# Kernel tuning notes

Hardware: AMD Instinct MI355X
Metric: run time of the kernel (lower is better)

## Reference

```python
import jax, jax.numpy as jnp
import numpy as np

N = 50000      # nodes
E = 400000     # edges (before self-loops)
IN = 128       # in_channels
OUT = 64       # out_channels (per-head; concat=False averages heads)
HEADS = 8      # heads of first GAT layer; second layer has 1 head
NEG_SLOPE = 0.2


def _glorot(key, shape, fan_in, fan_out):
    s = jnp.sqrt(2.0 / (fan_in + fan_out)).astype(jnp.float32)
    return jax.random.normal(key, shape, jnp.float32) * s


def setup_inputs() -> dict:
    key = jax.random.key(0)
    ks = jax.random.split(key, 10)
    x = jax.random.normal(ks[0], (N, IN), jnp.float32)
    edge_index = jax.random.randint(ks[1], (2, E), 0, N)
    # layer 1: heads=HEADS, per-head dim OUT
    W1 = _glorot(ks[2], (IN, HEADS * OUT), IN, HEADS * OUT)
    att_src1 = _glorot(ks[3], (HEADS, OUT), OUT, 1)
    att_dst1 = _glorot(ks[4], (HEADS, OUT), OUT, 1)
    b1 = jnp.zeros((OUT,), jnp.float32)
    # layer 2: heads=1
    W2 = _glorot(ks[5], (OUT, 1 * OUT), OUT, OUT)
    att_src2 = _glorot(ks[6], (1, OUT), OUT, 1)
    att_dst2 = _glorot(ks[7], (1, OUT), OUT, 1)
    b2 = jnp.zeros((OUT,), jnp.float32)
    return dict(x=x, edge_index=edge_index, W1=W1, att_src1=att_src1,
                att_dst1=att_dst1, b1=b1, W2=W2, att_src2=att_src2,
                att_dst2=att_dst2, b2=b2)


def gat_conv(x, edge_index, W, att_src, att_dst, bias, heads, ch):
    """PyG GATConv with concat=False (mean over heads), add_self_loops=True."""
    n = x.shape[0]
    loop = jnp.arange(n, dtype=edge_index.dtype)
    src = jnp.concatenate([edge_index[0], loop])  # [E+N]
    dst = jnp.concatenate([edge_index[1], loop])
    h = (x @ W).reshape(n, heads, ch)                     # [N, H, C]
    a_s = jnp.sum(h * att_src, axis=-1)                   # [N, H]
    a_d = jnp.sum(h * att_dst, axis=-1)                   # [N, H]
    e = jax.nn.leaky_relu(a_s[src] + a_d[dst], NEG_SLOPE)  # [E+N, H]
    # numerically stable segment softmax over incoming edges of each dst node
    emax = jax.lax.stop_gradient(
        jax.ops.segment_max(e, dst, num_segments=n))       # [N, H]
    ee = jnp.exp(e - emax[dst])
    denom = jax.ops.segment_sum(ee, dst, num_segments=n)  # [N, H]
    alpha = ee / denom[dst]                                # [E+N, H]
    out = jax.ops.segment_sum(alpha[:, :, None] * h[src], dst,
                              num_segments=n)              # [N, H, C]
    return out.mean(axis=1) + bias                         # [N, C]


def reference(x, edge_index, W1, att_src1, att_dst1, b1,
              W2, att_src2, att_dst2, b2):
    h = gat_conv(x, edge_index, W1, att_src1, att_dst1, b1, HEADS, OUT)
    h = jax.nn.elu(h)
    return gat_conv(h, edge_index, W2, att_src2, att_dst2, b2, 1, OUT)
```

## Files before the change

kernel.cpp:

```cpp
#include <hip/hip_runtime.h>
#include <cstdint>
#include <cstddef>

#define NEG_SLOPE 0.2f

typedef short bf16x8 __attribute__((ext_vector_type(8)));
typedef float f32x4 __attribute__((ext_vector_type(4)));
typedef float f32x2 __attribute__((ext_vector_type(2)));

__device__ __forceinline__ unsigned short f2bf(float f) {
  unsigned u = __float_as_uint(f);
  u = u + 0x7FFFu + ((u >> 16) & 1u);
  return (unsigned short)(u >> 16);
}
__device__ __forceinline__ float bf2f(unsigned short b) {
  return __uint_as_float((unsigned)b << 16);
}
__device__ __forceinline__ f32x2 unpk(unsigned xv) {
  f32x2 r;
  r.x = __uint_as_float(xv << 16);
  r.y = __uint_as_float(xv & 0xFFFF0000u);
  return r;
}
__device__ __forceinline__ void dma16(const unsigned short* g, unsigned short* l) {
  __builtin_amdgcn_global_load_lds(
      (const __attribute__((address_space(1))) unsigned*)g,
      (__attribute__((address_space(3))) unsigned*)l, 16, 0, 0);
}

__global__ __launch_bounds__(256) void prep_all(
    const int* __restrict__ ei, int* __restrict__ counts,
    const float* __restrict__ x, unsigned short* __restrict__ xb,
    const float* __restrict__ W1, const float* __restrict__ att_s1,
    const float* __restrict__ att_d1, unsigned short* __restrict__ AsAdT,
    unsigned short* __restrict__ WbT,
    const float* __restrict__ W2, unsigned short* __restrict__ W2t,
    const float* __restrict__ att_s2, const float* __restrict__ att_d2,
    float* __restrict__ AsAd2,
    int E, int ET, int N, int B0, int B1) {
  int b = blockIdx.x, tid = threadIdx.x;
  if (b < B0) {
    int i = b * 256 + tid;
    if (i < ET) {
      int dst = (i < E) ? ei[E + i] : (i - E);
      atomicAdd(&counts[dst], 1);
    }
    return;
  }
  b -= B0;
  if (b < B1) {
    int i = b * 256 + tid;
    if (i < N * 32) {
      float4 v = ((const float4*)x)[i];
      ushort4 o;
      o.x = f2bf(v.x); o.y = f2bf(v.y); o.z = f2bf(v.z); o.w = f2bf(v.w);
      ((ushort4*)xb)[i] = o;
    }
    return;
  }
  b -= B1;
  if (b < 8) {
    int i = b * 256 + tid;
    int o = i >> 7, k = i & 127, h = o & 7;
    const float* att = (o < 8) ? att_s1 : att_d1;
    float s = 0.f;
    for (int c = 0; c < 64; c++) s += W1[(size_t)k * 512 + h * 64 + c] * att[h * 64 + c];
    AsAdT[i] = f2bf(s);
    return;
  }
  b -= 8;
  if (b < 256) {
    int i = b * 256 + tid;
    int o = i >> 10, k = i & 1023, h = k >> 7, c = k & 127;
    WbT[i] = f2bf(W1[(size_t)c * 512 + h * 64 + o]);
    return;
  }
  b -= 256;
  if (b < 16) {
    int i = b * 256 + tid;
    if (i < 64 * 64) {
      int k = i >> 6, nn = i & 63;
      W2t[(size_t)nn * 64 + k] = f2bf(W2[i]);
    }
    return;
  }
  {
    int i = tid;
    if (i < 128) {
      int o = i >> 6, k = i & 63;
      const float* att = (o == 0) ? att_s2 : att_d2;
      float s = 0.f;
      for (int c = 0; c < 64; c++) s += W2[(size_t)k * 64 + c] * att[c];
      AsAd2[i] = s;
    }
  }
}

__global__ __launch_bounds__(1024) void scan_dots(
    const int* __restrict__ counts, int* __restrict__ offsets,
    const unsigned short* __restrict__ xb, const unsigned short* __restrict__ AsAdT,
    float* __restrict__ asd, int n) {
  if (blockIdx.x == 0) {
    __shared__ int sums[1024];
    int t = threadIdx.x;
    int chunk = (n + 1023) >> 10;
    int start = t * chunk;
    int end = min(start + chunk, n);
    int s = 0;
    for (int i = start; i < end; i++) s += counts[i];
    sums[t] = s;
    __syncthreads();
    for (int off = 1; off < 1024; off <<= 1) {
      int v = (t >= off) ? sums[t - off] : 0;
      __syncthreads();
      sums[t] += v;
      __syncthreads();
    }
    int run = sums[t] - s;
    for (int i = start; i < end; i++) { offsets[i] = run; run += counts[i]; }
    if (t == 1023) offsets[n] = sums[1023];
    return;
  }
  int tid = threadIdx.x;
  int wave = tid >> 6, lane = tid & 63;
  int q = lane >> 4, t = lane & 15;
  int row0 = (blockIdx.x - 1) * 256 + wave * 16;
  int arow = row0 + t; if (arow > n - 1) arow = n - 1;
  const bf16x8* aptr = (const bf16x8*)(xb + (size_t)arow * 128);
  const bf16x8* bptr = (const bf16x8*)(AsAdT + t * 128);
  f32x4 acc = (f32x4){0.f, 0.f, 0.f, 0.f};
  #pragma unroll
  for (int s = 0; s < 4; s++)
    acc = __builtin_amdgcn_mfma_f32_16x16x32_bf16(aptr[s * 4 + q], bptr[s * 4 + q],
                                                  acc, 0, 0, 0);
  #pragma unroll
  for (int r = 0; r < 4; r++) {
    int row = row0 + q * 4 + r;
    if (row < n) asd[row * 16 + t] = acc[r];
  }
}

__global__ __launch_bounds__(256) void fill_weights(
    const int* __restrict__ ei, const int* __restrict__ offsets,
    int* __restrict__ cursor, int* __restrict__ srcs,
    const float* __restrict__ asd, float* __restrict__ wbuf,
    int E, int ET) {
  int i = blockIdx.x * 256 + threadIdx.x;
  if (i >= ET) return;
  int src, dst;
  if (i < E) { src = ei[i]; dst = ei[E + i]; } else { src = dst = i - E; }
  int pos = atomicAdd(&cursor[dst], 1);
  int slot = offsets[dst] + pos;
  srcs[slot] = src;
  float4 s0 = *(const float4*)&asd[src * 16];
  float4 s1 = *(const float4*)&asd[src * 16 + 4];
  float4 d0 = *(const float4*)&asd[dst * 16 + 8];
  float4 d1 = *(const float4*)&asd[dst * 16 + 12];
  float w[8];
  w[0] = s0.x + d0.x; w[1] = s0.y + d0.y; w[2] = s0.z + d0.z; w[3] = s0.w + d0.w;
  w[4] = s1.x + d1.x; w[5] = s1.y + d1.y; w[6] = s1.z + d1.z; w[7] = s1.w + d1.w;
  #pragma unroll
  for (int h = 0; h < 8; h++) {
    float v = w[h];
    v = (v > 0.f) ? v : NEG_SLOPE * v;
    w[h] = __expf(v);
  }
  float4* wp = (float4*)&wbuf[(size_t)slot * 8];
  wp[0] = make_float4(w[0], w[1], w[2], w[3]);
  wp[1] = make_float4(w[4], w[5], w[6], w[7]);
}

__global__ __launch_bounds__(1024, 8) void agg1_gemm(
    const int* __restrict__ offsets, const int* __restrict__ srcs,
    const float* __restrict__ wbuf, const unsigned short* __restrict__ xb,
    const unsigned short* __restrict__ WbT, const float* __restrict__ b1,
    const float* __restrict__ AsAd2, unsigned short* __restrict__ zb,
    float* __restrict__ as2, float* __restrict__ ad2, int N) {
  __shared__ unsigned short sh[16 * 1032];
  __shared__ float sas[16], sad[16];
  int tid = threadIdx.x;
  int wv = tid >> 6, lane = tid & 63;
  int nb = blockIdx.x;
  {
    int row = wv;
    int node = nb * 16 + row;
    unsigned short* stg = &sh[row * 1032];
    f32x2 acc[8];
    float ws[8];
    #pragma unroll
    for (int h = 0; h < 8; h++) { acc[h] = (f32x2){0.f, 0.f}; ws[h] = 0.f; }
    int beg = offsets[node], end = offsets[node + 1];
    int jl = end - 1;
    int e0 = min(beg + (lane >> 4), jl);
    int e1 = min(beg + 4 + (lane >> 4), jl);
    int s0 = srcs[e0], s1 = srcs[e1];
    int we = min(beg + (lane >> 3), jl);
    float wl = wbuf[(size_t)we * 8 + (lane & 7)];
    for (int cb = beg; cb < end; cb += 8) {
      dma16(xb + (size_t)s0 * 128 + (lane & 15) * 8, stg);
      dma16(xb + (size_t)s1 * 128 + (lane & 15) * 8, stg + 512);
      float wcur = wl;
      int cn = cb + 8;
      int e0n = min(cn + (lane >> 4), jl);
      int e1n = min(cn + 4 + (lane >> 4), jl);
      s0 = srcs[e0n];
      s1 = srcs[e1n];
      int wen = min(cn + (lane >> 3), jl);
      wl = wbuf[(size_t)wen * 8 + (lane & 7)];
      __builtin_amdgcn_s_waitcnt(0x0f70);
      int cnt = min(8, end - cb);
      for (int k = 0; k < cnt; k++) {
        float w0 = __shfl(wcur, k * 8 + 0, 64);
        float w1 = __shfl(wcur, k * 8 + 1, 64);
        float w2 = __shfl(wcur, k * 8 + 2, 64);
        float w3 = __shfl(wcur, k * 8 + 3, 64);
        float w4 = __shfl(wcur, k * 8 + 4, 64);
        float w5 = __shfl(wcur, k * 8 + 5, 64);
        float w6 = __shfl(wcur, k * 8 + 6, 64);
        float w7 = __shfl(wcur, k * 8 + 7, 64);
        unsigned xv = *(const unsigned*)&stg[k * 128 + 2 * lane];
        f32x2 x2 = unpk(xv);
        acc[0] += x2 * w0; ws[0] += w0;
        acc[1] += x2 * w1; ws[1] += w1;
        acc[2] += x2 * w2; ws[2] += w2;
        acc[3] += x2 * w3; ws[3] += w3;
        acc[4] += x2 * w4; ws[4] += w4;
        acc[5] += x2 * w5; ws[5] += w5;
        acc[6] += x2 * w6; ws[6] += w6;
        acc[7] += x2 * w7; ws[7] += w7;
      }
    }
    #pragma unroll
    for (int h = 0; h < 8; h++) {
      float iv = 0.125f / ws[h];
      unsigned o = (unsigned)f2bf(acc[h].x * iv) | ((unsigned)f2bf(acc[h].y * iv) << 16);
      *(unsigned*)&sh[row * 1032 + h * 128 + 2 * lane] = o;
    }
  }
  if (tid < 16) sas[tid] = 0.f;
  else if (tid < 32) sad[tid - 16] = 0.f;
  __syncthreads();
  if (wv < 4) {
    int q = lane >> 4, t = lane & 15;
    f32x4 acc4 = (f32x4){0.f, 0.f, 0.f, 0.f};
    const unsigned short* bbase = WbT + (size_t)(wv * 16 + t) * 1024;
    #pragma unroll 8
    for (int s = 0; s < 32; s++) {
      bf16x8 af = *(const bf16x8*)&sh[t * 1032 + s * 32 + q * 8];
      bf16x8 bf = *(const bf16x8*)&bbase[s * 32 + q * 8];
      acc4 = __builtin_amdgcn_mfma_f32_16x16x32_bf16(af, bf, acc4, 0, 0, 0);
    }
    int col = wv * 16 + t;
    float bias = b1[col];
    float vs = AsAd2[col], vd = AsAd2[64 + col];
    float zr[4];
    #pragma unroll
    for (int r = 0; r < 4; r++) {
      int row = q * 4 + r;
      int node = nb * 16 + row;
      float v = acc4[r] + bias;
      v = (v > 0.f) ? v : (__expf(v) - 1.f);
      zr[r] = v;
      zb[(size_t)node * 64 + col] = f2bf(v);
    }
    #pragma unroll
    for (int r = 0; r < 4; r++) {
      float s = zr[r] * vs, d = zr[r] * vd;
      #pragma unroll
      for (int off = 1; off < 16; off <<= 1) {
        s += __shfl_xor(s, off, 64);
        d += __shfl_xor(d, off, 64);
      }
      if (t == 0) {
        atomicAdd(&sas[q * 4 + r], s);
        atomicAdd(&sad[q * 4 + r], d);
      }
    }
  }
  __syncthreads();
  if (tid < 16) as2[nb * 16 + tid] = sas[tid];
  else if (tid < 32) ad2[nb * 16 + (tid - 16)] = sad[tid - 16];
}

__global__ __launch_bounds__(1024, 8) void agg2_gemm(
    const int* __restrict__ offsets, const int* __restrict__ srcs,
    const float* __restrict__ as2, const float* __restrict__ ad2,
    const unsigned short* __restrict__ zb, const unsigned short* __restrict__ W2t,
    const float* __restrict__ b2, float* __restrict__ out, int N) {
  __shared__ unsigned short sh[16 * 72];
  __shared__ int ssrc[16][64];
  int tid = threadIdx.x;
  int wv = tid >> 6, lane = tid & 63;
  int nb = blockIdx.x;
  {
    int row = wv;
    int node = nb * 16 + row;
    int half = lane >> 5;
    int l2 = lane & 31;
    float adv = ad2[node];
    int beg = offsets[node], end = offsets[node + 1];
    f32x2 acc = (f32x2){0.f, 0.f};
    float ws = 0.f;
    for (int cb = beg; cb < end; cb += 64) {
      int cnt = min(64, end - cb);
      if (lane < cnt) ssrc[row][lane] = srcs[cb + lane];
      #pragma unroll 2
      for (int k = half; k < cnt; k += 2) {
        int s = ssrc[row][k];
        float asv = as2[s];
        unsigned zv = *(const unsigned*)&zb[(size_t)s * 64 + 2 * l2];
        float v = asv + adv;
        v = (v > 0.f) ? v : NEG_SLOPE * v;
        float w = __expf(v);
        ws += w;
        acc += unpk(zv) * w;
      }
    }
    acc.x += __shfl_xor(acc.x, 32, 64);
    acc.y += __shfl_xor(acc.y, 32, 64);
    ws += __shfl_xor(ws, 32, 64);
    if (half == 0) {
      float inv = 1.f / ws;
      unsigned o = (unsigned)f2bf(acc.x * inv) | ((unsigned)f2bf(acc.y * inv) << 16);
      *(unsigned*)&sh[row * 72 + 2 * l2] = o;
    }
  }
  __syncthreads();
  if (wv < 4) {
    int q = lane >> 4, t = lane & 15;
    f32x4 acc4 = (f32x4){0.f, 0.f, 0.f, 0.f};
    const unsigned short* bbase = W2t + (size_t)(wv * 16 + t) * 64;
    #pragma unroll
    for (int s = 0; s < 2; s++) {
      bf16x8 af = *(const bf16x8*)&sh[t * 72 + s * 32 + q * 8];
      bf16x8 bf = *(const bf16x8*)&bbase[s * 32 + q * 8];
      acc4 = __builtin_amdgcn_mfma_f32_16x16x32_bf16(af, bf, acc4, 0, 0, 0);
    }
    int col = wv * 16 + t;
    float bias = b2[col];
    #pragma unroll
    for (int r = 0; r < 4; r++) {
      int node = nb * 16 + q * 4 + r;
      if (node < N) out[(size_t)node * 64 + col] = acc4[r] + bias;
    }
  }
}

extern "C" void kernel_launch(void* const* d_in, const int* in_sizes, int n_in,
                              void* d_out, int out_size, void* d_ws, size_t ws_size,
                              hipStream_t stream) {
  const int IN = 128;
  const int N = in_sizes[0] / IN;
  const int E = in_sizes[1] / 2;
  const int ET = E + N;

  const float* x        = (const float*)d_in[0];
  const int*   ei       = (const int*)d_in[1];
  const float* W1       = (const float*)d_in[2];
  const float* att_src1 = (const float*)d_in[3];
  const float* att_dst1 = (const float*)d_in[4];
  const float* b1       = (const float*)d_in[5];
  const float* W2       = (const float*)d_in[6];
  const float* att_src2 = (const float*)d_in[7];
  const float* att_dst2 = (const float*)d_in[8];
  const float* b2       = (const float*)d_in[9];
  float* out = (float*)d_out;

  char* base = (char*)d_ws;
  size_t off = 0;
  auto alloc = [&](size_t bytes) -> char* {
    char* p = base + off;
    off = (off + bytes + 255) & ~(size_t)255;
    return p;
  };
  unsigned short* xb    = (unsigned short*)alloc((size_t)N * 128 * 2);
  unsigned short* AsAdT = (unsigned short*)alloc((size_t)16 * 128 * 2);
  unsigned short* WbT   = (unsigned short*)alloc((size_t)64 * 1024 * 2);
  unsigned short* W2t   = (unsigned short*)alloc((size_t)64 * 64 * 2);
  unsigned short* zb    = (unsigned short*)alloc((size_t)N * 64 * 2);
  float* AsAd2 = (float*)alloc((size_t)128 * 4);
  float* asd1  = (float*)alloc((size_t)N * 16 * 4);
  float* a_s2  = (float*)alloc((size_t)N * 4);
  float* a_d2  = (float*)alloc((size_t)N * 4);
  float* wbuf  = (float*)alloc((size_t)ET * 8 * 4);
  int* offsets = (int*)alloc((size_t)(N + 1) * 4);
  int* srcs    = (int*)alloc((size_t)ET * 4);
  char* zero_begin = base + off;
  int* counts  = (int*)alloc((size_t)N * 4);
  int* cursor  = (int*)alloc((size_t)N * 4);
  char* zero_end = base + off;

  hipMemsetAsync(zero_begin, 0, (size_t)(zero_end - zero_begin), stream);

  const int TB = 256;
  auto cdiv = [](int a, int b) { return (a + b - 1) / b; };

  int B0 = cdiv(ET, TB);
  int B1 = cdiv(N * 32, TB);
  prep_all<<<B0 + B1 + 8 + 256 + 16 + 1, TB, 0, stream>>>(
      ei, counts, x, xb, W1, att_src1, att_dst1, AsAdT, WbT, W2, W2t,
      att_src2, att_dst2, AsAd2, E, ET, N, B0, B1);

  scan_dots<<<1 + cdiv(N, 256), 1024, 0, stream>>>(counts, offsets, xb, AsAdT,
                                                   asd1, N);

  fill_weights<<<cdiv(ET, TB), TB, 0, stream>>>(ei, offsets, cursor, srcs,
                                                asd1, wbuf, E, ET);

  agg1_gemm<<<cdiv(N, 16), 1024, 0, stream>>>(offsets, srcs, wbuf, xb, WbT, b1,
                                              AsAd2, zb, a_s2, a_d2, N);

  agg2_gemm<<<cdiv(N, 16), 1024, 0, stream>>>(offsets, srcs, a_s2, a_d2, zb,
                                              W2t, b2, out, N);
}
```

Measured before the change: 339.7 us.

## Fuse edge-weight computation into layer-1 aggregation and process 16 edges per iteration

The per-edge attention weights (leaky-relu plus exp) are no longer precomputed and stored in a separate buffer. The layer-1 aggregation kernel now computes them on the fly from the per-node score table, so the weight buffer write and read disappear and the CSR fill kernel only scatters source indices. The aggregation loop now stages 16 neighbours per iteration through a larger shared buffer, broadcasts weights with readlane, and sums the softmax denominators with a final cross-lane reduction. Layer-2 scores are accumulated with global atomics into zeroed arrays instead of shared-memory atomics, and the larger shared allocation may lower occupancy.

```diff
diff --git a/kernel.cpp b/kernel.cpp
--- a/kernel.cpp
+++ b/kernel.cpp
@@ -21,6 +21,10 @@
   r.x = __uint_as_float(xv << 16);
   r.y = __uint_as_float(xv & 0xFFFF0000u);
   return r;
+}
+__device__ __forceinline__ float rlf(float v, int l) {
+  return __uint_as_float(
+      (unsigned)__builtin_amdgcn_readlane((int)__float_as_uint(v), l));
 }
 __device__ __forceinline__ void dma16(const unsigned short* g, unsigned short* l) {
   __builtin_amdgcn_global_load_lds(
@@ -140,105 +144,127 @@
   }
 }
 
-__global__ __launch_bounds__(256) void fill_weights(
+__global__ __launch_bounds__(256) void fill_csr(
     const int* __restrict__ ei, const int* __restrict__ offsets,
-    int* __restrict__ cursor, int* __restrict__ srcs,
-    const float* __restrict__ asd, float* __restrict__ wbuf,
-    int E, int ET) {
+    int* __restrict__ cursor, int* __restrict__ srcs, int E, int ET) {
   int i = blockIdx.x * 256 + threadIdx.x;
   if (i >= ET) return;
   int src, dst;
   if (i < E) { src = ei[i]; dst = ei[E + i]; } else { src = dst = i - E; }
   int pos = atomicAdd(&cursor[dst], 1);
-  int slot = offsets[dst] + pos;
-  srcs[slot] = src;
-  float4 s0 = *(const float4*)&asd[src * 16];
-  float4 s1 = *(const float4*)&asd[src * 16 + 4];
-  float4 d0 = *(const float4*)&asd[dst * 16 + 8];
-  float4 d1 = *(const float4*)&asd[dst * 16 + 12];
-  float w[8];
-  w[0] = s0.x + d0.x; w[1] = s0.y + d0.y; w[2] = s0.z + d0.z; w[3] = s0.w + d0.w;
-  w[4] = s1.x + d1.x; w[5] = s1.y + d1.y; w[6] = s1.z + d1.z; w[7] = s1.w + d1.w;
-  #pragma unroll
-  for (int h = 0; h < 8; h++) {
-    float v = w[h];
-    v = (v > 0.f) ? v : NEG_SLOPE * v;
-    w[h] = __expf(v);
-  }
-  float4* wp = (float4*)&wbuf[(size_t)slot * 8];
-  wp[0] = make_float4(w[0], w[1], w[2], w[3]);
-  wp[1] = make_float4(w[4], w[5], w[6], w[7]);
+  srcs[offsets[dst] + pos] = src;
 }
 
 __global__ __launch_bounds__(1024, 8) void agg1_gemm(
     const int* __restrict__ offsets, const int* __restrict__ srcs,
-    const float* __restrict__ wbuf, const unsigned short* __restrict__ xb,
+    const float* __restrict__ asd, const unsigned short* __restrict__ xb,
     const unsigned short* __restrict__ WbT, const float* __restrict__ b1,
     const float* __restrict__ AsAd2, unsigned short* __restrict__ zb,
     float* __restrict__ as2, float* __restrict__ ad2, int N) {
-  __shared__ unsigned short sh[16 * 1032];
-  __shared__ float sas[16], sad[16];
+  __shared__ unsigned short sh[16 * 2048];
   int tid = threadIdx.x;
   int wv = tid >> 6, lane = tid & 63;
   int nb = blockIdx.x;
   {
-    int row = wv;
-    int node = nb * 16 + row;
-    unsigned short* stg = &sh[row * 1032];
+    int node = nb * 16 + wv;
+    unsigned short* stg = &sh[wv * 2048];
     f32x2 acc[8];
-    float ws[8];
     #pragma unroll
-    for (int h = 0; h < 8; h++) { acc[h] = (f32x2){0.f, 0.f}; ws[h] = 0.f; }
+    for (int h = 0; h < 8; h++) acc[h] = (f32x2){0.f, 0.f};
+    float wsl = 0.f;
     int beg = offsets[node], end = offsets[node + 1];
     int jl = end - 1;
-    int e0 = min(beg + (lane >> 4), jl);
-    int e1 = min(beg + 4 + (lane >> 4), jl);
-    int s0 = srcs[e0], s1 = srcs[e1];
-    int we = min(beg + (lane >> 3), jl);
-    float wl = wbuf[(size_t)we * 8 + (lane & 7)];
-    for (int cb = beg; cb < end; cb += 8) {
+    float adv = asd[(size_t)node * 16 + 8 + (lane & 7)];
+    int s0 = srcs[min(beg + (lane >> 4), jl)];
+    int s1 = srcs[min(beg + 4 + (lane >> 4), jl)];
+    int s2 = 0, s3 = 0;
+    float asva, asvb = 0.f;
+    {
+      int swa = srcs[min(beg + (lane >> 3), jl)];
+      asva = asd[(size_t)swa * 16 + (lane & 7)];
+    }
+    if (end - beg > 8) {
+      s2 = srcs[min(beg + 8 + (lane >> 4), jl)];
+      s3 = srcs[min(beg + 12 + (lane >> 4), jl)];
+      int swb = srcs[min(beg + 8 + (lane >> 3), jl)];
+      asvb = asd[(size_t)swb * 16 + (lane & 7)];
+    }
+    for (int cb = beg; cb < end; cb += 16) {
+      int rem = end - cb;
+      bool bigh = rem > 8;
       dma16(xb + (size_t)s0 * 128 + (lane & 15) * 8, stg);
       dma16(xb + (size_t)s1 * 128 + (lane & 15) * 8, stg + 512);
-      float wcur = wl;
-      int cn = cb + 8;
-      int e0n = min(cn + (lane >> 4), jl);
-      int e1n = min(cn + 4 + (lane >> 4), jl);
-      s0 = srcs[e0n];
-      s1 = srcs[e1n];
-      int wen = min(cn + (lane >> 3), jl);
-      wl = wbuf[(size_t)wen * 8 + (lane & 7)];
+      if (bigh) {
+        dma16(xb + (size_t)s2 * 128 + (lane & 15) * 8, stg + 1024);
+        dma16(xb + (size_t)s3 * 128 + (lane & 15) * 8, stg + 1536);
+      }
+      float wa, wb = 0.f;
+      {
+        float v = asva + adv;
+        v = (v > 0.f) ? v : NEG_SLOPE * v;
+        wa = (cb + (lane >> 3) < end) ? __expf(v) : 0.f;
+      }
+      if (bigh) {
+        float v = asvb + adv;
+        v = (v > 0.f) ? v : NEG_SLOPE * v;
+        wb = (cb + 8 + (lane >> 3) < end) ? __expf(v) : 0.f;
+      }
+      wsl += wa + wb;
+      int cn = cb + 16;
+      if (cn < end) {
+        s0 = srcs[min(cn + (lane >> 4), jl)];
+        s1 = srcs[min(cn + 4 + (lane >> 4), jl)];
+        int swa = srcs[min(cn + (lane >> 3), jl)];
+        asva = asd[(size_t)swa * 16 + (lane & 7)];
+        if (end - cn > 8) {
+          s2 = srcs[min(cn + 8 + (lane >> 4), jl)];
+          s3 = srcs[min(cn + 12 + (lane >> 4), jl)];
+          int swb = srcs[min(cn + 8 + (lane >> 3), jl)];
+          asvb = asd[(size_t)swb * 16 + (lane & 7)];
+        }
+      }
       __builtin_amdgcn_s_waitcnt(0x0f70);
-      int cnt = min(8, end - cb);
-      for (int k = 0; k < cnt; k++) {
-        float w0 = __shfl(wcur, k * 8 + 0, 64);
-        float w1 = __shfl(wcur, k * 8 + 1, 64);
-        float w2 = __shfl(wcur, k * 8 + 2, 64);
-        float w3 = __shfl(wcur, k * 8 + 3, 64);
-        float w4 = __shfl(wcur, k * 8 + 4, 64);
-        float w5 = __shfl(wcur, k * 8 + 5, 64);
-        float w6 = __shfl(wcur, k * 8 + 6, 64);
-        float w7 = __shfl(wcur, k * 8 + 7, 64);
+      #pragma unroll
+      for (int k = 0; k < 8; k++) {
         unsigned xv = *(const unsigned*)&stg[k * 128 + 2 * lane];
         f32x2 x2 = unpk(xv);
-        acc[0] += x2 * w0; ws[0] += w0;
-        acc[1] += x2 * w1; ws[1] += w1;
-        acc[2] += x2 * w2; ws[2] += w2;
-        acc[3] += x2 * w3; ws[3] += w3;
-        acc[4] += x2 * w4; ws[4] += w4;
-        acc[5] += x2 * w5; ws[5] += w5;
-        acc[6] += x2 * w6; ws[6] += w6;
-        acc[7] += x2 * w7; ws[7] += w7;
-      }
-    }
+        acc[0] += x2 * rlf(wa, k * 8 + 0);
+        acc[1] += x2 * rlf(wa, k * 8 + 1);
+        acc[2] += x2 * rlf(wa, k * 8 + 2);
+        acc[3] += x2 * rlf(wa, k * 8 + 3);
+        acc[4] += x2 * rlf(wa, k * 8 + 4);
+        acc[5] += x2 * rlf(wa, k * 8 + 5);
+        acc[6] += x2 * rlf(wa, k * 8 + 6);
+        acc[7] += x2 * rlf(wa, k * 8 + 7);
+      }
+      if (bigh) {
+        #pragma unroll
+        for (int k = 0; k < 8; k++) {
+          unsigned xv = *(const unsigned*)&stg[1024 + k * 128 + 2 * lane];
+          f32x2 x2 = unpk(xv);
+          acc[0] += x2 * rlf(wb, k * 8 + 0);
+          acc[1] += x2 * rlf(wb, k * 8 + 1);
+          acc[2] += x2 * rlf(wb, k * 8 + 2);
+          acc[3] += x2 * rlf(wb, k * 8 + 3);
+          acc[4] += x2 * rlf(wb, k * 8 + 4);
+          acc[5] += x2 * rlf(wb, k * 8 + 5);
+          acc[6] += x2 * rlf(wb, k * 8 + 6);
+          acc[7] += x2 * rlf(wb, k * 8 + 7);
+        }
+      }
+    }
+    wsl += __shfl_xor(wsl, 8, 64);
+    wsl += __shfl_xor(wsl, 16, 64);
+    wsl += __shfl_xor(wsl, 32, 64);
+    __syncthreads();
     #pragma unroll
     for (int h = 0; h < 8; h++) {
-      float iv = 0.125f / ws[h];
+      float tot = rlf(wsl, h);
+      float iv = 0.125f / tot;
       unsigned o = (unsigned)f2bf(acc[h].x * iv) | ((unsigned)f2bf(acc[h].y * iv) << 16);
-      *(unsigned*)&sh[row * 1032 + h * 128 + 2 * lane] = o;
-    }
-  }
-  if (tid < 16) sas[tid] = 0.f;
-  else if (tid < 32) sad[tid - 16] = 0.f;
+      *(unsigned*)&sh[wv * 1032 + h * 128 + 2 * lane] = o;
+    }
+  }
   __syncthreads();
   if (wv < 4) {
     int q = lane >> 4, t = lane & 15;
@@ -253,33 +279,25 @@
     int col = wv * 16 + t;
     float bias = b1[col];
     float vs = AsAd2[col], vd = AsAd2[64 + col];
-    float zr[4];
     #pragma unroll
     for (int r = 0; r < 4; r++) {
       int row = q * 4 + r;
       int node = nb * 16 + row;
       float v = acc4[r] + bias;
       v = (v > 0.f) ? v : (__expf(v) - 1.f);
-      zr[r] = v;
       zb[(size_t)node * 64 + col] = f2bf(v);
-    }
-    #pragma unroll
-    for (int r = 0; r < 4; r++) {
-      float s = zr[r] * vs, d = zr[r] * vd;
+      float s = v * vs, d = v * vd;
       #pragma unroll
       for (int off = 1; off < 16; off <<= 1) {
         s += __shfl_xor(s, off, 64);
         d += __shfl_xor(d, off, 64);
       }
       if (t == 0) {
-        atomicAdd(&sas[q * 4 + r], s);
-        atomicAdd(&sad[q * 4 + r], d);
-      }
-    }
-  }
-  __syncthreads();
-  if (tid < 16) as2[nb * 16 + tid] = sas[tid];
-  else if (tid < 32) ad2[nb * 16 + (tid - 16)] = sad[tid - 16];
+        atomicAdd(&as2[node], s);
+        atomicAdd(&ad2[node], d);
+      }
+    }
+  }
 }
 
 __global__ __launch_bounds__(1024, 8) void agg2_gemm(
@@ -380,14 +398,13 @@
   unsigned short* zb    = (unsigned short*)alloc((size_t)N * 64 * 2);
   float* AsAd2 = (float*)alloc((size_t)128 * 4);
   float* asd1  = (float*)alloc((size_t)N * 16 * 4);
-  float* a_s2  = (float*)alloc((size_t)N * 4);
-  float* a_d2  = (float*)alloc((size_t)N * 4);
-  float* wbuf  = (float*)alloc((size_t)ET * 8 * 4);
   int* offsets = (int*)alloc((size_t)(N + 1) * 4);
   int* srcs    = (int*)alloc((size_t)ET * 4);
   char* zero_begin = base + off;
   int* counts  = (int*)alloc((size_t)N * 4);
   int* cursor  = (int*)alloc((size_t)N * 4);
+  float* a_s2  = (float*)alloc((size_t)N * 4);
+  float* a_d2  = (float*)alloc((size_t)N * 4);
   char* zero_end = base + off;
 
   hipMemsetAsync(zero_begin, 0, (size_t)(zero_end - zero_begin), stream);
@@ -404,10 +421,9 @@
   scan_dots<<<1 + cdiv(N, 256), 1024, 0, stream>>>(counts, offsets, xb, AsAdT,
                                                    asd1, N);
 
-  fill_weights<<<cdiv(ET, TB), TB, 0, stream>>>(ei, offsets, cursor, srcs,
-                                                asd1, wbuf, E, ET);
-
-  agg1_gemm<<<cdiv(N, 16), 1024, 0, stream>>>(offsets, srcs, wbuf, xb, WbT, b1,
+  fill_csr<<<cdiv(ET, TB), TB, 0, stream>>>(ei, offsets, cursor, srcs, E, ET);
+
+  agg1_gemm<<<cdiv(N, 16), 1024, 0, stream>>>(offsets, srcs, asd1, xb, WbT, b1,
                                               AsAd2, zb, a_s2, a_d2, N);
 
   agg2_gemm<<<cdiv(N, 16), 1024, 0, stream>>>(offsets, srcs, a_s2, a_d2, zb,
```

Result: faster. 325.0 us (-4.3%).
